# Kernel tuning notes

Measured on AMD Instinct MI355X. Metric: run time of the kernel, lower is better.

The kernel has to match this reference:

```python
import jax, jax.numpy as jnp
import numpy as np

N_NODES = 100000
N_EDGES = 3200000
N_GRAPHS = 512


def setup_inputs() -> dict:
    key = jax.random.key(0)
    k1, k2, k3, k4, k5 = jax.random.split(key, 5)
    x = jax.random.normal(k1, (N_NODES, 5), dtype=jnp.float32)
    edge_index = jax.random.randint(k2, (2, N_EDGES), 0, N_NODES, dtype=jnp.int64)
    batch = jnp.sort(jax.random.randint(k3, (N_NODES,), 0, N_GRAPHS, dtype=jnp.int64))
    W1 = jax.random.normal(k4, (5, 16), dtype=jnp.float32) * (1.0 / np.sqrt(5.0))
    b1 = jnp.zeros((16,), dtype=jnp.float32)
    W2 = jax.random.normal(k5, (16, 16), dtype=jnp.float32) * 0.25
    b2 = jnp.zeros((16,), dtype=jnp.float32)
    return {"x": x, "edge_index": edge_index, "batch": batch,
            "W1": W1, "b1": b1, "W2": W2, "b2": b2}


def _gcn_conv(x, src, dst, norm, W, b, n_nodes):
    # PyG GCNConv: h = X W; out_i = sum_{j->i} norm_ij * h_j + b
    h = x @ W                                   # [N, out]
    msgs = h[src] * norm[:, None]               # gather + scale  [E_tot, out]
    out = jax.ops.segment_sum(msgs, dst, num_segments=n_nodes)
    return out + b


def reference(x, edge_index, batch, W1, b1, W2, b2):
    n = x.shape[0]
    # add self-loops (GCNConv default)
    loops = jnp.arange(n, dtype=edge_index.dtype)
    src = jnp.concatenate([edge_index[0], loops])
    dst = jnp.concatenate([edge_index[1], loops])
    # symmetric normalization: deg computed on destination nodes
    deg = jax.ops.segment_sum(jnp.ones_like(src, dtype=x.dtype), dst, num_segments=n)
    dinv = jnp.where(deg > 0, jax.lax.rsqrt(deg), 0.0)
    norm = dinv[src] * dinv[dst]                # [E_tot]

    h = jax.nn.relu(_gcn_conv(x, src, dst, norm, W1, b1, n))
    h = jax.nn.relu(_gcn_conv(h, src, dst, norm, W2, b2, n))

    # global mean pool over graphs in the batch
    sums = jax.ops.segment_sum(h, batch, num_segments=N_GRAPHS)
    cnts = jax.ops.segment_sum(jnp.ones((n,), dtype=h.dtype), batch, num_segments=N_GRAPHS)
    return sums / jnp.maximum(cnts, 1.0)[:, None]
```

## Files before the change

kernel.cpp:

```cpp
#include <hip/hip_runtime.h>

#define N_NODES  100000
#define N_EDGES  3200000
#define N_GRAPHS 512
#define F_IN     5
#define F_HID    16

#define PBLK   512
#define CHUNK  4096
#define NBLK   ((N_EDGES + CHUNK - 1) / CHUNK)
#define BKT_NODES 256
#define NBKT ((N_NODES + BKT_NODES - 1) / BKT_NODES)
#define HPAD   512
#define CAP    10240


__device__ inline unsigned short f2bf(float f) {
    unsigned u = __float_as_uint(f);
    return (unsigned short)((u + 0x7fffu + ((u >> 16) & 1u)) >> 16);
}
__device__ inline float bf2f(unsigned short h) {
    return __uint_as_float(((unsigned)h) << 16);
}
__device__ inline float4 cvt4(ushort4 u) {
    return make_float4(bf2f(u.x), bf2f(u.y), bf2f(u.z), bf2f(u.w));
}
__device__ inline float4 shfl_xor4(float4 v, int m) {
    return make_float4(__shfl_xor(v.x, m, 64), __shfl_xor(v.y, m, 64),
                       __shfl_xor(v.z, m, 64), __shfl_xor(v.w, m, 64));
}

template <int NW>
__device__ inline int block_incl_scan(int v, int t, int* wsum) {
    int lane = t & 63, wave = t >> 6;
    int x = v;
#pragma unroll
    for (int o = 1; o < 64; o <<= 1) {
        int y = __shfl_up(x, o, 64);
        if (lane >= o) x += y;
    }
    if (lane == 63) wsum[wave] = x;
    __syncthreads();
    if (t < 64) {
        int w = (t < NW) ? wsum[t] : 0;
#pragma unroll
        for (int o = 1; o < NW; o <<= 1) {
            int y = __shfl_up(w, o, 64);
            if (t >= o) w += y;
        }
        if (t < NW) wsum[t] = w;
    }
    __syncthreads();
    return x + (wave ? wsum[wave - 1] : 0);
}

__device__ inline float4 row_gather8s(const ushort4* __restrict__ pb4, int i, int j,
                                      int half, int beg, int len,
                                      const int* __restrict__ col) {
    float4 acc = half ? make_float4(0.f, 0.f, 0.f, 0.f)
                      : cvt4(pb4[i * 4 + j]);
    for (int k = half * 8; k < len; k += 16) {
        int4 c0 = *(const int4*)(col + beg + k);
        int4 c1 = *(const int4*)(col + beg + k + 4);
        ushort4 a0 = pb4[c0.x * 4 + j], a1 = pb4[c0.y * 4 + j];
        ushort4 a2 = pb4[c0.z * 4 + j], a3 = pb4[c0.w * 4 + j];
        ushort4 a4 = pb4[c1.x * 4 + j], a5 = pb4[c1.y * 4 + j];
        ushort4 a6 = pb4[c1.z * 4 + j], a7 = pb4[c1.w * 4 + j];
        float4 f0 = cvt4(a0), f1 = cvt4(a1), f2 = cvt4(a2), f3 = cvt4(a3);
        float4 f4 = cvt4(a4), f5 = cvt4(a5), f6 = cvt4(a6), f7 = cvt4(a7);
        acc.x += ((f0.x + f1.x) + (f2.x + f3.x)) + ((f4.x + f5.x) + (f6.x + f7.x));
        acc.y += ((f0.y + f1.y) + (f2.y + f3.y)) + ((f4.y + f5.y) + (f6.y + f7.y));
        acc.z += ((f0.z + f1.z) + (f2.z + f3.z)) + ((f4.z + f5.z) + (f6.z + f7.z));
        acc.w += ((f0.w + f1.w) + (f2.w + f3.w)) + ((f4.w + f5.w) + (f6.w + f7.w));
    }
    return acc;
}


__global__ void k_zero(float* __restrict__ out, float* __restrict__ cnt,
                       unsigned short* __restrict__ pb_a,
                       unsigned short* __restrict__ pb_b) {
    int i = blockIdx.x * blockDim.x + threadIdx.x;
    if (i < N_GRAPHS * F_HID) out[i] = 0.0f;
    if (i < N_GRAPHS) cnt[i] = 0.0f;
    if (i < F_HID) {
        pb_a[(size_t)N_NODES * F_HID + i] = 0;
        pb_b[(size_t)N_NODES * F_HID + i] = 0;
    }
}

__global__ __launch_bounds__(PBLK) void k_count(const int* __restrict__ dst,
                                                const int* __restrict__ batch,
                                                int* __restrict__ H,
                                                float* __restrict__ cnt) {
    __shared__ int hist[HPAD];
    __shared__ int bcnt[8];
    __shared__ int g0s;
    int t = threadIdx.x, blk = blockIdx.x;
    int chunk0 = blk * CHUNK;
    int n4 = min(CHUNK, N_EDGES - chunk0) >> 2;
    hist[t] = 0;
    if (t < 8) bcnt[t] = 0;
    if (t == 0 && blk < NBKT) {
        int nb = blk * BKT_NODES;
        g0s = batch[nb < N_NODES ? nb : N_NODES - 1];
    }
    __syncthreads();
    const int4* d4 = (const int4*)(dst + chunk0);
#pragma unroll
    for (int i = 0; i < CHUNK / 4 / PBLK; i++) {
        int k = t + i * PBLK;
        if (k < n4) {
            int4 d = d4[k];
            atomicAdd(&hist[d.x >> 8], 1);
            atomicAdd(&hist[d.y >> 8], 1);
            atomicAdd(&hist[d.z >> 8], 1);
            atomicAdd(&hist[d.w >> 8], 1);
        }
    }
    if (blk < NBKT && t < BKT_NODES) {
        int i2 = blk * BKT_NODES + t;
        if (i2 < N_NODES) {
            int g = batch[i2];
            int l = g - g0s;
            if (l >= 0 && l < 8) atomicAdd(&bcnt[l], 1);
            else atomicAdd(&cnt[g], 1.0f);
        }
    }
    __syncthreads();
    H[blk * HPAD + t] = hist[t];
    if (blk < NBKT && t < 8 && bcnt[t] > 0) atomicAdd(&cnt[g0s + t], (float)bcnt[t]);
}

__global__ __launch_bounds__(256) void k_scan(int* __restrict__ H,
                                              int* __restrict__ cnt_b) {
    __shared__ int wsum[8];
    int b = blockIdx.x, t = threadIdx.x;
    int v[4];
    int s = 0;
#pragma unroll
    for (int i = 0; i < 4; i++) {
        int pos = t * 4 + i;
        v[i] = (pos < NBLK) ? H[pos * HPAD + b] : 0;
        s += v[i];
    }
    int incl = block_incl_scan<4>(s, t, wsum);
    int run = incl - s;
#pragma unroll
    for (int i = 0; i < 4; i++) {
        int pos = t * 4 + i;
        if (pos < NBLK) H[pos * HPAD + b] = run;
        run += v[i];
    }
    if (t == 255) cnt_b[b] = incl;
}

__global__ __launch_bounds__(PBLK) void k_scatter(const int* __restrict__ src,
                                                  const int* __restrict__ dst,
                                                  const int* __restrict__ H,
                                                  unsigned* __restrict__ packed) {
    __shared__ int hist[HPAD];
    __shared__ int scn[HPAD];
    __shared__ int rnk[HPAD];
    __shared__ int base[HPAD];
    __shared__ int wsum[8];
    __shared__ unsigned pkd[CHUNK];
    __shared__ unsigned short bkt[CHUNK];
    int t = threadIdx.x, blk = blockIdx.x;
    int chunk0 = blk * CHUNK;
    int n = min(CHUNK, N_EDGES - chunk0);
    int n4 = n >> 2;
    hist[t] = 0;
    base[t] = H[blk * HPAD + t];
    __syncthreads();
    const int4* s4 = (const int4*)(src + chunk0);
    const int4* d4 = (const int4*)(dst + chunk0);
    int4 lsv[CHUNK / 4 / PBLK], ldv[CHUNK / 4 / PBLK];
#pragma unroll
    for (int i = 0; i < CHUNK / 4 / PBLK; i++) {
        int k = t + i * PBLK;
        if (k < n4) {
            lsv[i] = s4[k];
            ldv[i] = d4[k];
            atomicAdd(&hist[ldv[i].x >> 8], 1);
            atomicAdd(&hist[ldv[i].y >> 8], 1);
            atomicAdd(&hist[ldv[i].z >> 8], 1);
            atomicAdd(&hist[ldv[i].w >> 8], 1);
        }
    }
    __syncthreads();
    int v = hist[t];
    int incl = block_incl_scan<8>(v, t, wsum);
    int excl = incl - v;
    scn[t] = excl;
    rnk[t] = excl;
    __syncthreads();
#pragma unroll
    for (int i = 0; i < CHUNK / 4 / PBLK; i++) {
        int k = t + i * PBLK;
        if (k < n4) {
            int ds0 = ldv[i].x, ds1 = ldv[i].y, ds2 = ldv[i].z, ds3 = ldv[i].w;
            int ss0 = lsv[i].x, ss1 = lsv[i].y, ss2 = lsv[i].z, ss3 = lsv[i].w;
            int b0 = ds0 >> 8, b1 = ds1 >> 8, b2 = ds2 >> 8, b3 = ds3 >> 8;
            int r0 = atomicAdd(&rnk[b0], 1);
            pkd[r0] = ((unsigned)ss0 << 8) | (unsigned)(ds0 & 255);
            bkt[r0] = (unsigned short)b0;
            int r1 = atomicAdd(&rnk[b1], 1);
            pkd[r1] = ((unsigned)ss1 << 8) | (unsigned)(ds1 & 255);
            bkt[r1] = (unsigned short)b1;
            int r2 = atomicAdd(&rnk[b2], 1);
            pkd[r2] = ((unsigned)ss2 << 8) | (unsigned)(ds2 & 255);
            bkt[r2] = (unsigned short)b2;
            int r3 = atomicAdd(&rnk[b3], 1);
            pkd[r3] = ((unsigned)ss3 << 8) | (unsigned)(ds3 & 255);
            bkt[r3] = (unsigned short)b3;
        }
    }
    __syncthreads();
    for (int p = t; p < n; p += PBLK) {
        int b = bkt[p];
        packed[(size_t)b * CAP + base[b] + (p - scn[b])] = pkd[p];
    }
}

__global__ __launch_bounds__(1024) void k_csr(const int* __restrict__ cnt_b,
                                              const unsigned* __restrict__ packed,
                                              const float* __restrict__ x,
                                              const float* __restrict__ W1,
                                              int2* __restrict__ rowbc,
                                              int* __restrict__ col,
                                              float* __restrict__ dinv,
                                              unsigned short* __restrict__ pb) {
    __shared__ int hist[BKT_NODES];
    __shared__ int rnk[BKT_NODES];
    __shared__ int wsum[16];
    __shared__ int tots;
    __shared__ float w1[F_IN * F_HID];
    __shared__ unsigned pkd[CAP];
    int b = blockIdx.x, t = threadIdx.x;
    int base = b * CAP;
    if (t < BKT_NODES) hist[t] = 0;
    if (t == 0) tots = min(cnt_b[b], CAP);
    if (t >= 1024 - F_IN * F_HID) w1[t - (1024 - F_IN * F_HID)] = W1[t - (1024 - F_IN * F_HID)];
    __syncthreads();
    int tot = tots;
    const unsigned* pk = packed + (size_t)b * CAP;
    for (int k = t; k < tot; k += 1024) {
        unsigned u = pk[k];
        pkd[k] = u;
        atomicAdd(&hist[u & 255], 1);
    }
    __syncthreads();
    int v = (t < BKT_NODES) ? hist[t] : 0;
    int len = (v + 7) & ~7;
    int incl = block_incl_scan<16>(len, t, wsum);
    int excl = incl - len;
    if (t < BKT_NODES) rnk[t] = excl;
    __syncthreads();
    for (int e = t; e < tot; e += 1024) {
        unsigned w = pkd[e];
        int r = atomicAdd(&rnk[w & 255], 1);
        if (r < CAP) col[base + r] = (int)(w >> 8);
    }
    if (t < BKT_NODES) {
        int node = b * BKT_NODES + t;
        if (node < N_NODES) {
            int mylen = min(len, ((CAP - min(excl, CAP)) & ~7));
            for (int q = v; q < mylen; q++) {
                int r = excl + q;
                if (r < CAP) col[base + r] = N_NODES;
            }
            rowbc[node] = make_int2(base + excl, mylen);
            float di = rsqrtf((float)(1 + v));
            dinv[node] = di;
            float xi[F_IN];
#pragma unroll
            for (int k = 0; k < F_IN; k++) xi[k] = x[node * F_IN + k];
            float hv[F_HID];
#pragma unroll
            for (int c = 0; c < F_HID; c++) {
                float h = 0.0f;
#pragma unroll
                for (int k = 0; k < F_IN; k++) h += xi[k] * w1[k * F_HID + c];
                hv[c] = h * di;
            }
            unsigned pkk[8];
#pragma unroll
            for (int q = 0; q < 8; q++)
                pkk[q] = (unsigned)f2bf(hv[2 * q]) | ((unsigned)f2bf(hv[2 * q + 1]) << 16);
            uint4* d4 = (uint4*)(pb + (size_t)node * F_HID);
            d4[0] = make_uint4(pkk[0], pkk[1], pkk[2], pkk[3]);
            d4[1] = make_uint4(pkk[4], pkk[5], pkk[6], pkk[7]);
        }
    }
}

__global__ __launch_bounds__(256) void k_pull_mid(const int2* __restrict__ rowbc,
                                                  const int* __restrict__ col,
                                                  const unsigned short* __restrict__ pb,
                                                  const float* __restrict__ dinv,
                                                  const float* __restrict__ W2,
                                                  const float* __restrict__ b1,
                                                  unsigned short* __restrict__ pb2) {
    __shared__ float w[F_HID * F_HID];
    __shared__ float bb[F_HID];
    int t = threadIdx.x;
    w[t] = W2[t];
    if (t < F_HID) bb[t] = b1[t];
    __syncthreads();
    int gid = blockIdx.x * 256 + t;
    int i = gid >> 3;
    int half = (gid >> 2) & 1;
    int j = gid & 3;
    int2 rc = rowbc[i];
    float4 acc = row_gather8s((const ushort4*)pb, i, j, half, rc.x, rc.y, col);
    acc.x += __shfl_xor(acc.x, 4, 64);
    acc.y += __shfl_xor(acc.y, 4, 64);
    acc.z += __shfl_xor(acc.z, 4, 64);
    acc.w += __shfl_xor(acc.w, 4, 64);
    float di = dinv[i];
    float4 mine;
    mine.x = fmaxf(di * acc.x + bb[4 * j + 0], 0.0f);
    mine.y = fmaxf(di * acc.y + bb[4 * j + 1], 0.0f);
    mine.z = fmaxf(di * acc.z + bb[4 * j + 2], 0.0f);
    mine.w = fmaxf(di * acc.w + bb[4 * j + 3], 0.0f);
    float4 o1 = shfl_xor4(mine, 1);
    float4 o2 = shfl_xor4(mine, 2);
    float4 o3 = shfl_xor4(mine, 3);
    float4 hq0 = (j == 0) ? mine : ((j == 1) ? o1 : ((j == 2) ? o2 : o3));
    float4 hq1 = (j == 1) ? mine : ((j == 0) ? o1 : ((j == 3) ? o2 : o3));
    float4 hq2 = (j == 2) ? mine : ((j == 3) ? o1 : ((j == 0) ? o2 : o3));
    float4 hq3 = (j == 3) ? mine : ((j == 2) ? o1 : ((j == 1) ? o2 : o3));
    float hc[F_HID] = {hq0.x, hq0.y, hq0.z, hq0.w, hq1.x, hq1.y, hq1.z, hq1.w,
                       hq2.x, hq2.y, hq2.z, hq2.w, hq3.x, hq3.y, hq3.z, hq3.w};
    float m0 = 0.0f, m1 = 0.0f, m2 = 0.0f, m3 = 0.0f;
#pragma unroll
    for (int c = 0; c < F_HID; c++) {
        float4 wv = *(const float4*)&w[c * F_HID + 4 * j];
        float hv = hc[c];
        m0 += hv * wv.x; m1 += hv * wv.y; m2 += hv * wv.z; m3 += hv * wv.w;
    }
    if (half == 0) {
        unsigned p0 = (unsigned)f2bf(m0 * di) | ((unsigned)f2bf(m1 * di) << 16);
        unsigned p1 = (unsigned)f2bf(m2 * di) | ((unsigned)f2bf(m3 * di) << 16);
        *(uint2*)(pb2 + (size_t)i * F_HID + 4 * j) = make_uint2(p0, p1);
    }
}

__global__ __launch_bounds__(256) void k_pull_pool(const int2* __restrict__ rowbc,
                                                   const int* __restrict__ col,
                                                   const unsigned short* __restrict__ pb,
                                                   const float* __restrict__ dinv,
                                                   const int* __restrict__ batch,
                                                   const float* __restrict__ b2,
                                                   const float* __restrict__ cnt,
                                                   float* __restrict__ out) {
    __shared__ float bb[F_HID];
    __shared__ float acc2[8][F_HID];
    __shared__ int gcnt[8];
    __shared__ int g0s;
    int t = threadIdx.x;
    if (t < F_HID) bb[t] = b2[t];
    if (t < 8) gcnt[t] = 0;
    if (t < 8 * F_HID) ((float*)acc2)[t] = 0.0f;
    int blk0node = blockIdx.x * 32;
    if (t == 0) g0s = batch[blk0node < N_NODES ? blk0node : N_NODES - 1];
    __syncthreads();
    int g0 = g0s;
    int gid = blockIdx.x * 256 + t;
    int i = gid >> 3;
    int half = (gid >> 2) & 1;
    int j = gid & 3;
    int2 rc = rowbc[i];
    float4 acc = row_gather8s((const ushort4*)pb, i, j, half, rc.x, rc.y, col);
    acc.x += __shfl_xor(acc.x, 4, 64);
    acc.y += __shfl_xor(acc.y, 4, 64);
    acc.z += __shfl_xor(acc.z, 4, 64);
    acc.w += __shfl_xor(acc.w, 4, 64);
    if (half == 0) {
        float di = dinv[i];
        float h0 = fmaxf(di * acc.x + bb[4 * j + 0], 0.0f);
        float h1 = fmaxf(di * acc.y + bb[4 * j + 1], 0.0f);
        float h2 = fmaxf(di * acc.z + bb[4 * j + 2], 0.0f);
        float h3 = fmaxf(di * acc.w + bb[4 * j + 3], 0.0f);
        int g = batch[i];
        int l = g - g0;
        if (l >= 0 && l < 8) {
            atomicAdd(&acc2[l][4 * j + 0], h0);
            atomicAdd(&acc2[l][4 * j + 1], h1);
            atomicAdd(&acc2[l][4 * j + 2], h2);
            atomicAdd(&acc2[l][4 * j + 3], h3);
            if (j == 0) atomicAdd(&gcnt[l], 1);
        } else {
            float inv = 1.0f / cnt[g];
            atomicAdd(&out[g * F_HID + 4 * j + 0], h0 * inv);
            atomicAdd(&out[g * F_HID + 4 * j + 1], h1 * inv);
            atomicAdd(&out[g * F_HID + 4 * j + 2], h2 * inv);
            atomicAdd(&out[g * F_HID + 4 * j + 3], h3 * inv);
        }
    }
    __syncthreads();
    if (t < 8 * F_HID) {
        int l = t >> 4, c = t & 15;
        if (gcnt[l] > 0) {
            float inv = 1.0f / cnt[g0 + l];
            atomicAdd(&out[(g0 + l) * F_HID + c], acc2[l][c] * inv);
        }
    }
}


extern "C" void kernel_launch(void* const* d_in, const int* in_sizes, int n_in,
                              void* d_out, int out_size, void* d_ws, size_t ws_size,
                              hipStream_t stream) {
    const float* x     = (const float*)d_in[0];
    const int*   ei    = (const int*)d_in[1];
    const int*   batch = (const int*)d_in[2];
    const float* W1    = (const float*)d_in[3];
    const float* b1    = (const float*)d_in[4];
    const float* W2    = (const float*)d_in[5];
    const float* b2    = (const float*)d_in[6];
    float* out = (float*)d_out;

    int*            H      = (int*)d_ws;
    int*            cnt_b  = H + (size_t)NBLK * HPAD;
    unsigned*       packed = (unsigned*)(cnt_b + 512);
    int2*           rowbc  = (int2*)(packed + (size_t)NBKT * CAP);
    int*            col    = (int*)(rowbc + N_NODES);
    float*          dinv   = (float*)(col + (size_t)NBKT * CAP);
    unsigned short* pb_a   = (unsigned short*)(dinv + N_NODES);
    unsigned short* pb_b   = pb_a + (size_t)(N_NODES + 1) * F_HID;
    float*          cnt    = (float*)(pb_b + (size_t)(N_NODES + 1) * F_HID);

    const int* src = ei;
    const int* dst = ei + N_EDGES;

    const int nb_pull = (N_NODES * 8) / 256;

    k_zero<<<(N_GRAPHS * F_HID + 255) / 256, 256, 0, stream>>>(out, cnt, pb_a, pb_b);
    k_count<<<NBLK, PBLK, 0, stream>>>(dst, batch, H, cnt);
    k_scan<<<NBKT, 256, 0, stream>>>(H, cnt_b);
    k_scatter<<<NBLK, PBLK, 0, stream>>>(src, dst, H, packed);
    k_csr<<<NBKT, 1024, 0, stream>>>(cnt_b, packed, x, W1, rowbc, col, dinv, pb_a);
    k_pull_mid<<<nb_pull, 256, 0, stream>>>(rowbc, col, pb_a, dinv, W2, b1, pb_b);
    k_pull_pool<<<nb_pull, 256, 0, stream>>>(rowbc, col, pb_b, dinv, batch, b2,
                                             cnt, out);
}
```

Measured before the change: 173.8 us.

## Aggregate 5-wide input features before applying W1 in first GCN layer

Layer one now aggregates the dinv-scaled 5-feature inputs (bf16, one 16-byte row per node) over neighbours, then applies W1, bias, ReLU and W2 after the gather, using the linearity of the convolution. This shrinks each gathered row from 16 bf16 features to 5, reducing random-gather traffic in the first pull kernel. Each node is now handled by 4 threads with a strided edge loop and shuffle reduction instead of the previous 8-lane gather helper. The cost is an extra small 5x16 matmul per node and changed lane mapping, which may reduce memory-level parallelism per edge.

```diff
diff --git a/kernel.cpp b/kernel.cpp
--- a/kernel.cpp
+++ b/kernel.cpp
@@ -13,6 +13,8 @@
 #define NBKT ((N_NODES + BKT_NODES - 1) / BKT_NODES)
 #define HPAD   512
 #define CAP    10240
+#define PN1    64
+#define NPB1   ((N_NODES + PN1 - 1) / PN1)
 
 
 __device__ inline unsigned short f2bf(float f) {
@@ -28,6 +30,11 @@
 __device__ inline float4 shfl_xor4(float4 v, int m) {
     return make_float4(__shfl_xor(v.x, m, 64), __shfl_xor(v.y, m, 64),
                        __shfl_xor(v.z, m, 64), __shfl_xor(v.w, m, 64));
+}
+__device__ inline void unpack5(uint4 r0, float* f) {
+    f[0] = bf2f((unsigned short)r0.x); f[1] = bf2f((unsigned short)(r0.x >> 16));
+    f[2] = bf2f((unsigned short)r0.y); f[3] = bf2f((unsigned short)(r0.y >> 16));
+    f[4] = bf2f((unsigned short)r0.z);
 }
 
 template <int NW>
@@ -83,10 +90,8 @@
     int i = blockIdx.x * blockDim.x + threadIdx.x;
     if (i < N_GRAPHS * F_HID) out[i] = 0.0f;
     if (i < N_GRAPHS) cnt[i] = 0.0f;
-    if (i < F_HID) {
-        pb_a[(size_t)N_NODES * F_HID + i] = 0;
-        pb_b[(size_t)N_NODES * F_HID + i] = 0;
-    }
+    if (i < 8)  pb_a[(size_t)N_NODES * 8 + i] = 0;
+    if (i < F_HID) pb_b[(size_t)N_NODES * F_HID + i] = 0;
 }
 
 __global__ __launch_bounds__(PBLK) void k_count(const int* __restrict__ dst,
@@ -226,7 +231,6 @@
 __global__ __launch_bounds__(1024) void k_csr(const int* __restrict__ cnt_b,
                                               const unsigned* __restrict__ packed,
                                               const float* __restrict__ x,
-                                              const float* __restrict__ W1,
                                               int2* __restrict__ rowbc,
                                               int* __restrict__ col,
                                               float* __restrict__ dinv,
@@ -235,13 +239,11 @@
     __shared__ int rnk[BKT_NODES];
     __shared__ int wsum[16];
     __shared__ int tots;
-    __shared__ float w1[F_IN * F_HID];
     __shared__ unsigned pkd[CAP];
     int b = blockIdx.x, t = threadIdx.x;
     int base = b * CAP;
     if (t < BKT_NODES) hist[t] = 0;
     if (t == 0) tots = min(cnt_b[b], CAP);
-    if (t >= 1024 - F_IN * F_HID) w1[t - (1024 - F_IN * F_HID)] = W1[t - (1024 - F_IN * F_HID)];
     __syncthreads();
     int tot = tots;
     const unsigned* pk = packed + (size_t)b * CAP;
@@ -273,24 +275,14 @@
             rowbc[node] = make_int2(base + excl, mylen);
             float di = rsqrtf((float)(1 + v));
             dinv[node] = di;
-            float xi[F_IN];
-#pragma unroll
-            for (int k = 0; k < F_IN; k++) xi[k] = x[node * F_IN + k];
-            float hv[F_HID];
-#pragma unroll
-            for (int c = 0; c < F_HID; c++) {
-                float h = 0.0f;
-#pragma unroll
-                for (int k = 0; k < F_IN; k++) h += xi[k] * w1[k * F_HID + c];
-                hv[c] = h * di;
-            }
-            unsigned pkk[8];
-#pragma unroll
-            for (int q = 0; q < 8; q++)
-                pkk[q] = (unsigned)f2bf(hv[2 * q]) | ((unsigned)f2bf(hv[2 * q + 1]) << 16);
-            uint4* d4 = (uint4*)(pb + (size_t)node * F_HID);
-            d4[0] = make_uint4(pkk[0], pkk[1], pkk[2], pkk[3]);
-            d4[1] = make_uint4(pkk[4], pkk[5], pkk[6], pkk[7]);
+            float xd[6];
+#pragma unroll
+            for (int k = 0; k < F_IN; k++) xd[k] = x[node * F_IN + k] * di;
+            xd[5] = 0.0f;
+            unsigned p0 = (unsigned)f2bf(xd[0]) | ((unsigned)f2bf(xd[1]) << 16);
+            unsigned p1 = (unsigned)f2bf(xd[2]) | ((unsigned)f2bf(xd[3]) << 16);
+            unsigned p2 = (unsigned)f2bf(xd[4]);
+            *(uint4*)(pb + (size_t)node * 8) = make_uint4(p0, p1, p2, 0u);
         }
     }
 }
@@ -299,51 +291,59 @@
                                                   const int* __restrict__ col,
                                                   const unsigned short* __restrict__ pb,
                                                   const float* __restrict__ dinv,
+                                                  const float* __restrict__ W1,
                                                   const float* __restrict__ W2,
                                                   const float* __restrict__ b1,
                                                   unsigned short* __restrict__ pb2) {
-    __shared__ float w[F_HID * F_HID];
-    __shared__ float bb[F_HID];
+    __shared__ float w2[F_HID * F_HID];
+    __shared__ float w1s[F_IN * F_HID];
+    __shared__ float b1s[F_HID];
     int t = threadIdx.x;
-    w[t] = W2[t];
-    if (t < F_HID) bb[t] = b1[t];
-    __syncthreads();
-    int gid = blockIdx.x * 256 + t;
-    int i = gid >> 3;
-    int half = (gid >> 2) & 1;
-    int j = gid & 3;
-    int2 rc = rowbc[i];
-    float4 acc = row_gather8s((const ushort4*)pb, i, j, half, rc.x, rc.y, col);
-    acc.x += __shfl_xor(acc.x, 4, 64);
-    acc.y += __shfl_xor(acc.y, 4, 64);
-    acc.z += __shfl_xor(acc.z, 4, 64);
-    acc.w += __shfl_xor(acc.w, 4, 64);
-    float di = dinv[i];
-    float4 mine;
-    mine.x = fmaxf(di * acc.x + bb[4 * j + 0], 0.0f);
-    mine.y = fmaxf(di * acc.y + bb[4 * j + 1], 0.0f);
-    mine.z = fmaxf(di * acc.z + bb[4 * j + 2], 0.0f);
-    mine.w = fmaxf(di * acc.w + bb[4 * j + 3], 0.0f);
-    float4 o1 = shfl_xor4(mine, 1);
-    float4 o2 = shfl_xor4(mine, 2);
-    float4 o3 = shfl_xor4(mine, 3);
-    float4 hq0 = (j == 0) ? mine : ((j == 1) ? o1 : ((j == 2) ? o2 : o3));
-    float4 hq1 = (j == 1) ? mine : ((j == 0) ? o1 : ((j == 3) ? o2 : o3));
-    float4 hq2 = (j == 2) ? mine : ((j == 3) ? o1 : ((j == 0) ? o2 : o3));
-    float4 hq3 = (j == 3) ? mine : ((j == 2) ? o1 : ((j == 1) ? o2 : o3));
-    float hc[F_HID] = {hq0.x, hq0.y, hq0.z, hq0.w, hq1.x, hq1.y, hq1.z, hq1.w,
-                       hq2.x, hq2.y, hq2.z, hq2.w, hq3.x, hq3.y, hq3.z, hq3.w};
-    float m0 = 0.0f, m1 = 0.0f, m2 = 0.0f, m3 = 0.0f;
-#pragma unroll
-    for (int c = 0; c < F_HID; c++) {
-        float4 wv = *(const float4*)&w[c * F_HID + 4 * j];
-        float hv = hc[c];
-        m0 += hv * wv.x; m1 += hv * wv.y; m2 += hv * wv.z; m3 += hv * wv.w;
-    }
-    if (half == 0) {
+    w2[t] = W2[t];
+    if (t < F_IN * F_HID) w1s[t] = W1[t];
+    if (t < F_HID) b1s[t] = b1[t];
+    __syncthreads();
+    int nl = t >> 2, q = t & 3;
+    int node = blockIdx.x * PN1 + nl;
+    const uint4* pbx = (const uint4*)pb;
+    float f5[F_IN];
+#pragma unroll
+    for (int c = 0; c < F_IN; c++) f5[c] = 0.0f;
+    if (node < N_NODES) {
+        int2 rc = rowbc[node];
+        if (q == 0) unpack5(pbx[node], f5);
+        for (int i = q; i < rc.y; i += 4) {
+            int s = col[rc.x + i];
+            float g[F_IN];
+            unpack5(pbx[s], g);
+#pragma unroll
+            for (int c = 0; c < F_IN; c++) f5[c] += g[c];
+        }
+    }
+#pragma unroll
+    for (int c = 0; c < F_IN; c++) {
+        f5[c] += __shfl_xor(f5[c], 1, 64);
+        f5[c] += __shfl_xor(f5[c], 2, 64);
+    }
+    if (node < N_NODES) {
+        float di = dinv[node];
+        float h[F_HID];
+#pragma unroll
+        for (int c = 0; c < F_HID; c++) {
+            float s = 0.0f;
+#pragma unroll
+            for (int k = 0; k < F_IN; k++) s += f5[k] * w1s[k * F_HID + c];
+            h[c] = fmaxf(di * s + b1s[c], 0.0f);
+        }
+        float m0 = 0.0f, m1 = 0.0f, m2 = 0.0f, m3 = 0.0f;
+#pragma unroll
+        for (int c = 0; c < F_HID; c++) {
+            float4 wv = *(const float4*)&w2[c * F_HID + 4 * q];
+            m0 += h[c] * wv.x; m1 += h[c] * wv.y; m2 += h[c] * wv.z; m3 += h[c] * wv.w;
+        }
         unsigned p0 = (unsigned)f2bf(m0 * di) | ((unsigned)f2bf(m1 * di) << 16);
         unsigned p1 = (unsigned)f2bf(m2 * di) | ((unsigned)f2bf(m3 * di) << 16);
-        *(uint2*)(pb2 + (size_t)i * F_HID + 4 * j) = make_uint2(p0, p1);
+        *(uint2*)(pb2 + (size_t)node * F_HID + 4 * q) = make_uint2(p0, p1);
     }
 }
 
@@ -435,14 +435,14 @@
     const int* src = ei;
     const int* dst = ei + N_EDGES;
 
-    const int nb_pull = (N_NODES * 8) / 256;
+    const int nb_pull2 = (N_NODES * 8) / 256;
 
     k_zero<<<(N_GRAPHS * F_HID + 255) / 256, 256, 0, stream>>>(out, cnt, pb_a, pb_b);
     k_count<<<NBLK, PBLK, 0, stream>>>(dst, batch, H, cnt);
     k_scan<<<NBKT, 256, 0, stream>>>(H, cnt_b);
     k_scatter<<<NBLK, PBLK, 0, stream>>>(src, dst, H, packed);
-    k_csr<<<NBKT, 1024, 0, stream>>>(cnt_b, packed, x, W1, rowbc, col, dinv, pb_a);
-    k_pull_mid<<<nb_pull, 256, 0, stream>>>(rowbc, col, pb_a, dinv, W2, b1, pb_b);
-    k_pull_pool<<<nb_pull, 256, 0, stream>>>(rowbc, col, pb_b, dinv, batch, b2,
-                                             cnt, out);
-}
+    k_csr<<<NBKT, 1024, 0, stream>>>(cnt_b, packed, x, rowbc, col, dinv, pb_a);
+    k_pull_mid<<<NPB1, 256, 0, stream>>>(rowbc, col, pb_a, dinv, W1, W2, b1, pb_b);
+    k_pull_pool<<<nb_pull2, 256, 0, stream>>>(rowbc, col, pb_b, dinv, batch, b2,
+                                              cnt, out);
+}
```

Result: no change. 176.9 us (+1.8%).
